# Optimization experiments

Measured on AMD Instinct MI355X. Metric: run time of the kernel, lower is better.

Reference implementation:

```python
import jax, jax.numpy as jnp
import numpy as np

N_NODES = 50000
N_EDGES = 640000
IN_CH = 128
HIDDEN = 128
HEADS = 4
HEAD_DIM = HIDDEN // HEADS  # 32
NEG_SLOPE = 0.2


def setup_inputs() -> dict:
    key = jax.random.key(0)
    ks = jax.random.split(key, 12)
    x = jax.random.normal(ks[0], (N_NODES, IN_CH), dtype=jnp.float32)
    edge_index = jax.random.randint(ks[1], (2, N_EDGES), 0, N_NODES, dtype=jnp.int64)
    s = 0.1
    W1 = jax.random.normal(ks[2], (IN_CH, HEADS * HEAD_DIM), dtype=jnp.float32) * s
    a_src1 = jax.random.normal(ks[3], (HEADS, HEAD_DIM), dtype=jnp.float32) * s
    a_dst1 = jax.random.normal(ks[4], (HEADS, HEAD_DIM), dtype=jnp.float32) * s
    b1 = jax.random.normal(ks[5], (HEADS * HEAD_DIM,), dtype=jnp.float32) * s
    W2 = jax.random.normal(ks[6], (HIDDEN, HEADS * HEAD_DIM), dtype=jnp.float32) * s
    a_src2 = jax.random.normal(ks[7], (HEADS, HEAD_DIM), dtype=jnp.float32) * s
    a_dst2 = jax.random.normal(ks[8], (HEADS, HEAD_DIM), dtype=jnp.float32) * s
    b2 = jax.random.normal(ks[9], (HEADS * HEAD_DIM,), dtype=jnp.float32) * s
    return {"x": x, "edge_index": edge_index, "W1": W1, "a_src1": a_src1,
            "a_dst1": a_dst1, "b1": b1, "W2": W2, "a_src2": a_src2,
            "a_dst2": a_dst2, "b2": b2}


def _gat_conv(x, src, dst, W, a_src, a_dst, b):
    """PyG GATConv (concat=True, add_self_loops already applied to src/dst)."""
    N = x.shape[0]
    H, C = a_src.shape
    h = (x @ W).reshape(N, H, C)                      # [N, H, C]
    alpha_s = jnp.einsum('nhc,hc->nh', h, a_src)      # [N, H]
    alpha_d = jnp.einsum('nhc,hc->nh', h, a_dst)      # [N, H]
    e = alpha_s[src] + alpha_d[dst]                   # [E, H]
    e = jnp.where(e > 0, e, NEG_SLOPE * e)            # leaky_relu(0.2)
    # segment softmax over destination nodes (every node has a self-loop)
    emax = jax.ops.segment_max(e, dst, num_segments=N)
    ee = jnp.exp(e - emax[dst])
    denom = jax.ops.segment_sum(ee, dst, num_segments=N)
    alpha = ee / (denom[dst] + 1e-16)                 # [E, H]
    out = jax.ops.segment_sum(h[src] * alpha[:, :, None], dst, num_segments=N)
    return out.reshape(N, H * C) + b


def reference(x, edge_index, W1, a_src1, a_dst1, b1, W2, a_src2, a_dst2, b2):
    N = x.shape[0]
    loops = jnp.arange(N, dtype=edge_index.dtype)
    src = jnp.concatenate([edge_index[0], loops])
    dst = jnp.concatenate([edge_index[1], loops])
    h = _gat_conv(x, src, dst, W1, a_src1, a_dst1, b1)
    h = jax.nn.relu(h)  # dropout is identity in eval mode
    out = _gat_conv(h, src, dst, W2, a_src2, a_dst2, b2)
    return out
```

## Files before the change

### kernel.cpp

```cpp
#include <hip/hip_runtime.h>
#include <hip/hip_bf16.h>
#include <hip/hip_fp16.h>

#define N_NODES 50000
#define N_EDGES 640000
#define E_TOT   690000
#define CH      128
#define GEMMB   782
#define EBLK    2048
#define NEB     337
#define NBUCK   196
#define MTP     344

typedef __attribute__((ext_vector_type(8))) short short8;
typedef __attribute__((ext_vector_type(4))) float float4v;

static __device__ __forceinline__ float bf2f(unsigned short u) {
  return __uint_as_float(((unsigned)u) << 16);
}
static __device__ __forceinline__ unsigned short f2bf(float f) {
  unsigned u = __float_as_uint(f);
  return (unsigned short)((u + 0x7fffu + ((u >> 16) & 1u)) >> 16);
}

__global__ void k_detect(const unsigned short* __restrict__ x16,
                         const unsigned int* __restrict__ eiw,
                         int* __restrict__ flags)
{
  __shared__ int sf32, si64;
  int t = threadIdx.x;
  if (t == 0) { sf32 = 0; si64 = 1; }
  __syncthreads();
  int bad = 0;
  for (int i = t; i < 4096; i += 256) {
    float v = bf2f(x16[i]);
    if (!(v == v) || fabsf(v) > 100.f) bad = 1;
  }
  if (bad) atomicOr(&sf32, 1);
  if (t < 128 && eiw[2 * t + 1] != 0u) atomicAnd(&si64, 0);
  __syncthreads();
  if (t == 0) { flags[0] = sf32; flags[1] = si64; }
}

static __device__ __forceinline__ void load_edge(const int* __restrict__ ei,
                                                 int e, int i64, int& s, int& d)
{
  if (e >= N_EDGES) { s = d = e - N_EDGES; return; }
  if (i64) { s = ei[2 * (size_t)e]; d = ei[2 * ((size_t)N_EDGES + e)]; }
  else     { s = ei[e];             d = ei[N_EDGES + e]; }
}

static __device__ __forceinline__ short8 load_bf8(const void* __restrict__ X,
                                                  size_t off, int f32)
{
  if (!f32) return *(const short8*)((const unsigned short*)X + off);
  const float4* p = (const float4*)((const float*)X + off);
  float4 u = p[0], v = p[1];
  short8 r;
  r[0] = (short)f2bf(u.x); r[1] = (short)f2bf(u.y);
  r[2] = (short)f2bf(u.z); r[3] = (short)f2bf(u.w);
  r[4] = (short)f2bf(v.x); r[5] = (short)f2bf(v.y);
  r[6] = (short)f2bf(v.z); r[7] = (short)f2bf(v.w);
  return r;
}

__global__ __launch_bounds__(256) void k_prep(
    const void* __restrict__ W1, const void* __restrict__ W2,
    const void* __restrict__ as1, const void* __restrict__ ad1,
    const void* __restrict__ as2, const void* __restrict__ ad2,
    unsigned short* __restrict__ Wt1, unsigned short* __restrict__ Wt2,
    unsigned short* __restrict__ Ba1, unsigned short* __restrict__ Ba2,
    const int* __restrict__ flags)
{
  int f32 = flags[0];
  int b = blockIdx.x, t = threadIdx.x;
  if (b < 8) {
    int g = b * 256 + t;
    int l = g >> 10;
    int rem = g & 1023;
    int k = rem >> 3, n = rem & 7;
    const void* W  = l ? W2 : W1;
    const void* av = (n < 4) ? (l ? as2 : as1) : (l ? ad2 : ad1);
    int h = n & 3;
    float sum = 0.f;
    for (int c = 0; c < 32; c++) {
      float w = f32 ? ((const float*)W)[k * 128 + h * 32 + c]
                    : bf2f(((const unsigned short*)W)[k * 128 + h * 32 + c]);
      float a = f32 ? ((const float*)av)[h * 32 + c]
                    : bf2f(((const unsigned short*)av)[h * 32 + c]);
      sum += w * a;
    }
    unsigned short* Ba = l ? Ba2 : Ba1;
    Ba[n * 128 + k] = f2bf(sum);
    Ba[(8 + (rem >> 7)) * 128 + (rem & 127)] = 0;
  } else {
    int b2 = b - 8;
    int l = b2 >> 7, c = b2 & 127;
    if (t < 128) {
      const void* W = l ? W2 : W1;
      unsigned short* Wt = l ? Wt2 : Wt1;
      Wt[c * 128 + t] = f32 ? f2bf(((const float*)W)[t * 128 + c])
                            : ((const unsigned short*)W)[t * 128 + c];
    }
  }
}

struct SmemG { unsigned short WB[144][136]; };

static __device__ __forceinline__ void gemm_body(
    SmemG& sm, int bx,
    const void* __restrict__ X,
    const unsigned short* __restrict__ Wt_g,
    const unsigned short* __restrict__ Ba_g,
    unsigned short* __restrict__ H, float* __restrict__ AS,
    float* __restrict__ AD, int nrows, int xf32)
{
  int tid = threadIdx.x;
#pragma unroll
  for (int i = 0; i < 8; i++) {
    int j = i * 256 + tid;
    int c = j >> 4, k8 = j & 15;
    short8 v = *(const short8*)(Wt_g + c * 128 + k8 * 8);
    *(short8*)&sm.WB[c][k8 * 8] = v;
  }
  {
    int n = tid >> 4, k8 = tid & 15;
    short8 v = *(const short8*)(Ba_g + n * 128 + k8 * 8);
    *(short8*)&sm.WB[128 + n][k8 * 8] = v;
  }
  __syncthreads();
  int wave = tid >> 6, lane = tid & 63;
  int rt = bx * 4 + wave;
  if (rt * 16 >= nrows) return;
  int R0 = rt * 16;
  int m = lane & 15, quad = lane >> 4;
  size_t abase = (size_t)(R0 + m) * CH + quad * 8;
  float4v acc[8];
  float4v accA = (float4v){0.f, 0.f, 0.f, 0.f};
#pragma unroll
  for (int t = 0; t < 8; t++) acc[t] = (float4v){0.f, 0.f, 0.f, 0.f};
#pragma unroll
  for (int kb = 0; kb < 4; kb++) {
    short8 a = load_bf8(X, abase + kb * 32, xf32);
#pragma unroll
    for (int ct = 0; ct < 8; ct++) {
      short8 b = *(const short8*)&sm.WB[ct * 16 + m][kb * 32 + quad * 8];
      acc[ct] = __builtin_amdgcn_mfma_f32_16x16x32_bf16(a, b, acc[ct], 0, 0, 0);
    }
    short8 bA = *(const short8*)&sm.WB[128 + m][kb * 32 + quad * 8];
    accA = __builtin_amdgcn_mfma_f32_16x16x32_bf16(a, bA, accA, 0, 0, 0);
  }
  int rbase = R0 + quad * 4;
#pragma unroll
  for (int ct = 0; ct < 8; ct++) {
    int col = ct * 16 + m;
#pragma unroll
    for (int r = 0; r < 4; r++)
      H[(size_t)(rbase + r) * CH + col] = __half_as_ushort(__float2half(acc[ct][r]));
  }
  if (m < 4) {
#pragma unroll
    for (int r = 0; r < 4; r++)
      AS[(size_t)(rbase + r) * 4 + m] = accA[r];
  } else if (m < 8) {
#pragma unroll
    for (int r = 0; r < 4; r++)
      AD[(size_t)(rbase + r) * 4 + (m - 4)] = accA[r];
  }
}

__global__ __launch_bounds__(256, 2) void k_gemm(
    const void* __restrict__ X,
    const unsigned short* __restrict__ Wt_g,
    const unsigned short* __restrict__ Ba_g,
    unsigned short* __restrict__ H, float* __restrict__ AS, float* __restrict__ AD,
    int nrows)
{
  __shared__ SmemG sm;
  gemm_body(sm, blockIdx.x, X, Wt_g, Ba_g, H, AS, AD, nrows, 0);
}

__global__ __launch_bounds__(256, 2) void k_gemm_hist(
    const void* __restrict__ X,
    const unsigned short* __restrict__ Wt_g,
    const unsigned short* __restrict__ Ba_g,
    unsigned short* __restrict__ H, float* __restrict__ AS, float* __restrict__ AD,
    int nrows, const int* __restrict__ ei, int* __restrict__ MT,
    const int* __restrict__ flags)
{
  __shared__ SmemG sm;
  __shared__ int hist[NBUCK];
  if (blockIdx.x >= GEMMB) {
    int b = blockIdx.x - GEMMB;
    int t = threadIdx.x;
    if (t < NBUCK) hist[t] = 0;
    __syncthreads();
    int i64 = flags[1];
    int base = b * EBLK;
#pragma unroll
    for (int k = 0; k < 8; k++) {
      int e = base + k * 256 + t;
      if (e < E_TOT) {
        int s, d;
        load_edge(ei, e, i64, s, d);
        atomicAdd(&hist[d >> 8], 1);
      }
    }
    __syncthreads();
    if (t < NBUCK) MT[t * MTP + b] = hist[t];
    return;
  }
  gemm_body(sm, blockIdx.x, X, Wt_g, Ba_g, H, AS, AD, nrows, flags[0]);
}

__global__ __launch_bounds__(512) void k_rowscan(int* __restrict__ MT,
                                                 int* __restrict__ T)
{
  __shared__ int sh[512];
  int q = blockIdx.x, t = threadIdx.x;
  int v = (t < NEB) ? MT[q * MTP + t] : 0;
  sh[t] = v;
  __syncthreads();
  for (int off = 1; off < 512; off <<= 1) {
    int u = (t >= off) ? sh[t - off] : 0;
    __syncthreads();
    sh[t] += u;
    __syncthreads();
  }
  if (t < NEB) MT[q * MTP + t] = sh[t] - v;
  if (t == NEB - 1) T[q] = sh[t];
}

__global__ __launch_bounds__(256) void k_bscan(const int* __restrict__ T,
                                               int* __restrict__ BB)
{
  __shared__ int sh[256];
  int t = threadIdx.x;
  int v = (t < NBUCK) ? T[t] : 0;
  sh[t] = v;
  __syncthreads();
  for (int off = 1; off < 256; off <<= 1) {
    int u = (t >= off) ? sh[t - off] : 0;
    __syncthreads();
    sh[t] += u;
    __syncthreads();
  }
  if (t < NBUCK) BB[t] = sh[t] - v;
  if (t == NBUCK - 1) BB[NBUCK] = sh[t];
}

__global__ __launch_bounds__(256) void k_bucket(
    const int* __restrict__ ei, const int* __restrict__ MT,
    const int* __restrict__ BB, int2* __restrict__ ebuf,
    const int* __restrict__ flags)
{
  __shared__ int cur[NBUCK];
  int b = blockIdx.x, t = threadIdx.x;
  if (t < NBUCK) cur[t] = BB[t] + MT[t * MTP + b];
  __syncthreads();
  int i64 = flags[1];
  int base = b * EBLK;
#pragma unroll
  for (int k = 0; k < 8; k++) {
    int e = base + k * 256 + t;
    if (e < E_TOT) {
      int s, d;
      load_edge(ei, e, i64, s, d);
      int pos = atomicAdd(&cur[d >> 8], 1);
      ebuf[pos] = make_int2(s, d);
    }
  }
}

__global__ __launch_bounds__(256) void k_fine(
    const int2* __restrict__ ebuf, const int* __restrict__ BB,
    int* __restrict__ row_ptr, int* __restrict__ deg,
    int* __restrict__ csr_src)
{
  __shared__ int cnt[256], sh[256], cur[256];
  int q = blockIdx.x, t = threadIdx.x;
  int lo = BB[q], hi = BB[q + 1];
  cnt[t] = 0;
  __syncthreads();
  for (int i = lo + t; i < hi; i += 256)
    atomicAdd(&cnt[ebuf[i].y & 255], 1);
  __syncthreads();
  int v = cnt[t];
  sh[t] = v;
  __syncthreads();
  for (int off = 1; off < 256; off <<= 1) {
    int u = (t >= off) ? sh[t - off] : 0;
    __syncthreads();
    sh[t] += u;
    __syncthreads();
  }
  int lp = sh[t] - v;
  int n = (q << 8) + t;
  if (n < N_NODES) { row_ptr[n] = lo + lp; deg[n] = v; }
  cur[t] = lo + lp;
  __syncthreads();
  for (int i = lo + t; i < hi; i += 256) {
    int2 p = ebuf[i];
    int slot = atomicAdd(&cur[p.y & 255], 1);
    csr_src[slot] = p.x;
  }
}

__global__ __launch_bounds__(256) void k_agg(
    const int* __restrict__ row_ptr, const int* __restrict__ deg,
    const int* __restrict__ csr_src,
    const __half* __restrict__ H,
    const float* __restrict__ AS, const float* __restrict__ AD,
    const void* __restrict__ b, void* __restrict__ Y,
    const int* __restrict__ flags, int layer)
{
  int tid = threadIdx.x;
  int node = blockIdx.x * 4 + (tid >> 6);
  if (node >= N_NODES) return;
  int lane = tid & 63;
  int h = lane >> 4;
  int c0 = 2 * lane;
  float adh = AD[(size_t)node * 4 + h];
  int start = row_ptr[node];
  int dg = deg[node];
  const __half2* __restrict__ H2 = (const __half2*)H;
  float accx = 0.f, accy = 0.f, den = 0.f;
  int j = 0;
  for (; j + 8 <= dg; j += 8) {
    int sI[8];
#pragma unroll
    for (int u = 0; u < 8; u++) sI[u] = csr_src[start + j + u];
    float eV[8];
#pragma unroll
    for (int u = 0; u < 8; u++) eV[u] = AS[(size_t)sI[u] * 4 + h] + adh;
    float2 vV[8];
#pragma unroll
    for (int u = 0; u < 8; u++) vV[u] = __half22float2(H2[(size_t)sI[u] * 64 + lane]);
#pragma unroll
    for (int u = 0; u < 8; u++) {
      float x = eV[u] > 0.f ? eV[u] : 0.2f * eV[u];
      float ex = __expf(x);
      accx += ex * vV[u].x;
      accy += ex * vV[u].y;
      den  += ex;
    }
  }
  for (; j + 4 <= dg; j += 4) {
    int sI[4];
#pragma unroll
    for (int u = 0; u < 4; u++) sI[u] = csr_src[start + j + u];
    float eV[4];
#pragma unroll
    for (int u = 0; u < 4; u++) eV[u] = AS[(size_t)sI[u] * 4 + h] + adh;
    float2 vV[4];
#pragma unroll
    for (int u = 0; u < 4; u++) vV[u] = __half22float2(H2[(size_t)sI[u] * 64 + lane]);
#pragma unroll
    for (int u = 0; u < 4; u++) {
      float x = eV[u] > 0.f ? eV[u] : 0.2f * eV[u];
      float ex = __expf(x);
      accx += ex * vV[u].x;
      accy += ex * vV[u].y;
      den  += ex;
    }
  }
  for (; j < dg; j++) {
    int s = csr_src[start + j];
    float e = AS[(size_t)s * 4 + h] + adh;
    float2 v = __half22float2(H2[(size_t)s * 64 + lane]);
    e = e > 0.f ? e : 0.2f * e;
    float ex = __expf(e);
    accx += ex * v.x;
    accy += ex * v.y;
    den  += ex;
  }
  float inv = 1.f / (den + 1e-16f);
  int f32 = flags[0];
  float b0 = f32 ? ((const float*)b)[c0]     : bf2f(((const unsigned short*)b)[c0]);
  float b1 = f32 ? ((const float*)b)[c0 + 1] : bf2f(((const unsigned short*)b)[c0 + 1]);
  float r0 = accx * inv + b0;
  float r1 = accy * inv + b1;
  size_t o = (size_t)node * CH + c0;
  if (layer == 1) {
    r0 = r0 > 0.f ? r0 : 0.f;
    r1 = r1 > 0.f ? r1 : 0.f;
    ushort2 w; w.x = f2bf(r0); w.y = f2bf(r1);
    *(ushort2*)((unsigned short*)Y + o) = w;
  } else if (f32) {
    float2 w; w.x = r0; w.y = r1;
    *(float2*)((float*)Y + o) = w;
  } else {
    ushort2 w; w.x = f2bf(r0); w.y = f2bf(r1);
    *(ushort2*)((unsigned short*)Y + o) = w;
  }
}

extern "C" void kernel_launch(void* const* d_in, const int* in_sizes, int n_in,
                              void* d_out, int out_size, void* d_ws, size_t ws_size,
                              hipStream_t stream)
{
  const void* x   = d_in[0];
  const int*  ei  = (const int*)d_in[1];
  const void* W1  = d_in[2];
  const void* as1 = d_in[3];
  const void* ad1 = d_in[4];
  const void* b1  = d_in[5];
  const void* W2  = d_in[6];
  const void* as2 = d_in[7];
  const void* ad2 = d_in[8];
  const void* b2  = d_in[9];

  char* ws = (char*)d_ws;
  unsigned short* H  = (unsigned short*)(ws);
  float*  AS         = (float*)(ws + 12800000);
  float*  AD         = (float*)(ws + 13600000);
  unsigned short* X2 = (unsigned short*)(ws + 14400000);
  int*    deg        = (int*)(ws + 27200000);
  int*    row_ptr    = (int*)(ws + 27400000);
  int*    csr_src    = (int*)(ws + 27600000);
  int*    MT         = (int*)(ws + 30360000);
  int*    T          = (int*)(ws + 30630000);
  int*    BB         = (int*)(ws + 30631000);
  int*    flags      = (int*)(ws + 30632000);
  int2*   ebuf       = (int2*)(ws + 30640000);
  unsigned short* Wt1 = (unsigned short*)(ws + 36160000);
  unsigned short* Wt2 = (unsigned short*)(ws + 36200000);
  unsigned short* Ba1 = (unsigned short*)(ws + 36240000);
  unsigned short* Ba2 = (unsigned short*)(ws + 36248000);

  const int agg_blocks = (N_NODES + 3) / 4;

  k_detect<<<1, 256, 0, stream>>>((const unsigned short*)x,
                                  (const unsigned int*)ei, flags);
  k_prep<<<264, 256, 0, stream>>>(W1, W2, as1, ad1, as2, ad2,
                                  Wt1, Wt2, Ba1, Ba2, flags);

  k_gemm_hist<<<GEMMB + NEB, 256, 0, stream>>>(
      x, Wt1, Ba1, H, AS, AD, N_NODES, ei, MT, flags);

  k_rowscan<<<NBUCK, 512, 0, stream>>>(MT, T);
  k_bscan  <<<1, 256, 0, stream>>>(T, BB);
  k_bucket <<<NEB, 256, 0, stream>>>(ei, MT, BB, ebuf, flags);
  k_fine   <<<NBUCK, 256, 0, stream>>>(ebuf, BB, row_ptr, deg, csr_src);

  k_agg<<<agg_blocks, 256, 0, stream>>>(row_ptr, deg, csr_src,
                                        (const __half*)H, AS, AD,
                                        b1, X2, flags, 1);

  k_gemm<<<GEMMB, 256, 0, stream>>>(X2, Wt2, Ba2, H, AS, AD, N_NODES);
  k_agg<<<agg_blocks, 256, 0, stream>>>(row_ptr, deg, csr_src,
                                        (const __half*)H, AS, AD,
                                        b2, d_out, flags, 2);
}
```

Baseline: 214.8 us.

## Split each node's edges across two half-wavefronts with 8-byte gathers

The aggregation kernel now splits each node's edge list between the two 32-lane halves of the wavefront. Each lane loads four fp16 channels (8 bytes) per edge instead of two. The partial sums are combined with a cross-half shuffle, and the separate unrolled remainder loops are replaced by a single predicated loop that clamps indices and masks out-of-range edges. This doubles the number of independent edge gathers in flight per wavefront, at the cost of wasted masked work on low-degree nodes and an extra shuffle reduction.

```diff
diff --git a/kernel.cpp b/kernel.cpp
--- a/kernel.cpp
+++ b/kernel.cpp
@@ -14,6 +14,7 @@
 
 typedef __attribute__((ext_vector_type(8))) short short8;
 typedef __attribute__((ext_vector_type(4))) float float4v;
+typedef __attribute__((ext_vector_type(4))) unsigned short us4;
 
 static __device__ __forceinline__ float bf2f(unsigned short u) {
   return __uint_as_float(((unsigned)u) << 16);
@@ -306,6 +307,8 @@
   }
 }
 
+struct h2x2 { __half2 a, b; };
+
 __global__ __launch_bounds__(256) void k_agg(
     const int* __restrict__ row_ptr, const int* __restrict__ deg,
     const int* __restrict__ csr_src,
@@ -318,80 +321,77 @@
   int node = blockIdx.x * 4 + (tid >> 6);
   if (node >= N_NODES) return;
   int lane = tid & 63;
-  int h = lane >> 4;
-  int c0 = 2 * lane;
+  int hw = lane >> 5, ln = lane & 31;
+  int h = ln >> 3;
+  int c0 = 4 * ln;
   float adh = AD[(size_t)node * 4 + h];
   int start = row_ptr[node];
   int dg = deg[node];
-  const __half2* __restrict__ H2 = (const __half2*)H;
-  float accx = 0.f, accy = 0.f, den = 0.f;
-  int j = 0;
-  for (; j + 8 <= dg; j += 8) {
-    int sI[8];
-#pragma unroll
-    for (int u = 0; u < 8; u++) sI[u] = csr_src[start + j + u];
+  const h2x2* __restrict__ H4 = (const h2x2*)H;
+  float a0 = 0.f, a1 = 0.f, a2 = 0.f, a3 = 0.f, den = 0.f;
+  for (int j = 0; j < dg; j += 16) {
+    int sI[8]; float pr[8];
+#pragma unroll
+    for (int u = 0; u < 8; u++) {
+      int e = j + 2 * u + hw;
+      int idx = e < dg ? e : dg - 1;
+      sI[u] = csr_src[start + idx];
+      pr[u] = e < dg ? 1.f : 0.f;
+    }
     float eV[8];
 #pragma unroll
     for (int u = 0; u < 8; u++) eV[u] = AS[(size_t)sI[u] * 4 + h] + adh;
-    float2 vV[8];
-#pragma unroll
-    for (int u = 0; u < 8; u++) vV[u] = __half22float2(H2[(size_t)sI[u] * 64 + lane]);
+    h2x2 hv[8];
+#pragma unroll
+    for (int u = 0; u < 8; u++) hv[u] = H4[(size_t)sI[u] * 32 + ln];
 #pragma unroll
     for (int u = 0; u < 8; u++) {
       float x = eV[u] > 0.f ? eV[u] : 0.2f * eV[u];
-      float ex = __expf(x);
-      accx += ex * vV[u].x;
-      accy += ex * vV[u].y;
-      den  += ex;
-    }
-  }
-  for (; j + 4 <= dg; j += 4) {
-    int sI[4];
-#pragma unroll
-    for (int u = 0; u < 4; u++) sI[u] = csr_src[start + j + u];
-    float eV[4];
-#pragma unroll
-    for (int u = 0; u < 4; u++) eV[u] = AS[(size_t)sI[u] * 4 + h] + adh;
-    float2 vV[4];
-#pragma unroll
-    for (int u = 0; u < 4; u++) vV[u] = __half22float2(H2[(size_t)sI[u] * 64 + lane]);
-#pragma unroll
-    for (int u = 0; u < 4; u++) {
-      float x = eV[u] > 0.f ? eV[u] : 0.2f * eV[u];
-      float ex = __expf(x);
-      accx += ex * vV[u].x;
-      accy += ex * vV[u].y;
-      den  += ex;
-    }
-  }
-  for (; j < dg; j++) {
-    int s = csr_src[start + j];
-    float e = AS[(size_t)s * 4 + h] + adh;
-    float2 v = __half22float2(H2[(size_t)s * 64 + lane]);
-    e = e > 0.f ? e : 0.2f * e;
-    float ex = __expf(e);
-    accx += ex * v.x;
-    accy += ex * v.y;
-    den  += ex;
-  }
+      float ex = __expf(x) * pr[u];
+      float2 f0 = __half22float2(hv[u].a);
+      float2 f1 = __half22float2(hv[u].b);
+      a0 += ex * f0.x;
+      a1 += ex * f0.y;
+      a2 += ex * f1.x;
+      a3 += ex * f1.y;
+      den += ex;
+    }
+  }
+  a0 += __shfl_xor(a0, 32);
+  a1 += __shfl_xor(a1, 32);
+  a2 += __shfl_xor(a2, 32);
+  a3 += __shfl_xor(a3, 32);
+  den += __shfl_xor(den, 32);
+  if (hw) return;
   float inv = 1.f / (den + 1e-16f);
   int f32 = flags[0];
-  float b0 = f32 ? ((const float*)b)[c0]     : bf2f(((const unsigned short*)b)[c0]);
-  float b1 = f32 ? ((const float*)b)[c0 + 1] : bf2f(((const unsigned short*)b)[c0 + 1]);
-  float r0 = accx * inv + b0;
-  float r1 = accy * inv + b1;
+  float b0, b1, b2, b3;
+  if (f32) {
+    const float* bp = (const float*)b;
+    b0 = bp[c0]; b1 = bp[c0 + 1]; b2 = bp[c0 + 2]; b3 = bp[c0 + 3];
+  } else {
+    const unsigned short* bp = (const unsigned short*)b;
+    b0 = bf2f(bp[c0]); b1 = bf2f(bp[c0 + 1]);
+    b2 = bf2f(bp[c0 + 2]); b3 = bf2f(bp[c0 + 3]);
+  }
+  float r0 = a0 * inv + b0;
+  float r1 = a1 * inv + b1;
+  float r2 = a2 * inv + b2;
+  float r3 = a3 * inv + b3;
   size_t o = (size_t)node * CH + c0;
   if (layer == 1) {
     r0 = r0 > 0.f ? r0 : 0.f;
     r1 = r1 > 0.f ? r1 : 0.f;
-    ushort2 w; w.x = f2bf(r0); w.y = f2bf(r1);
-    *(ushort2*)((unsigned short*)Y + o) = w;
+    r2 = r2 > 0.f ? r2 : 0.f;
+    r3 = r3 > 0.f ? r3 : 0.f;
+    us4 w; w.x = f2bf(r0); w.y = f2bf(r1); w.z = f2bf(r2); w.w = f2bf(r3);
+    *(us4*)((unsigned short*)Y + o) = w;
   } else if (f32) {
-    float2 w; w.x = r0; w.y = r1;
-    *(float2*)((float*)Y + o) = w;
+    float4 w; w.x = r0; w.y = r1; w.z = r2; w.w = r3;
+    *(float4*)((float*)Y + o) = w;
   } else {
-    ushort2 w; w.x = f2bf(r0); w.y = f2bf(r1);
-    *(ushort2*)((unsigned short*)Y + o) = w;
+    us4 w; w.x = f2bf(r0); w.y = f2bf(r1); w.z = f2bf(r2); w.w = f2bf(r3);
+    *(us4*)((unsigned short*)Y + o) = w;
   }
 }
 
```

Measured after the change: 217.8 us. No clear change (+1.4%).
